# Kernel optimization log

Measured on AMD Instinct MI355X. Metric: run time of the kernel, lower is better.

## Reference

```python
import jax, jax.numpy as jnp
import numpy as np

N_HEAD = 16
N_EMBED = 1024

def setup_inputs() -> dict:
    key = jax.random.key(0)
    ks = jax.random.split(key, 5)
    C = N_EMBED
    x = jax.random.normal(ks[0], (2, 2048, C), dtype=jnp.float32)
    # c_attn: Linear(C, 3C); c_proj: Linear(C, C). PyTorch Linear: y = x @ W.T + b
    w_attn = jax.random.normal(ks[1], (3 * C, C), dtype=jnp.float32) * (1.0 / np.sqrt(C))
    b_attn = jnp.zeros((3 * C,), dtype=jnp.float32)
    w_proj = jax.random.normal(ks[2], (C, C), dtype=jnp.float32) * (1.0 / np.sqrt(C))
    b_proj = jnp.zeros((C,), dtype=jnp.float32)
    return {"x": x, "w_attn": w_attn, "b_attn": b_attn, "w_proj": w_proj, "b_proj": b_proj}

def reference(x, w_attn, b_attn, w_proj, b_proj):
    B, T, C = x.shape
    H = N_HEAD
    D = C // H
    qkv = jnp.einsum('btc,fc->btf', x, w_attn) + b_attn  # [B,T,3C]
    q, k, v = jnp.split(qkv, 3, axis=-1)
    # [B,H,T,D]
    q = q.reshape(B, T, H, D).transpose(0, 2, 1, 3)
    k = k.reshape(B, T, H, D).transpose(0, 2, 1, 3)
    v = v.reshape(B, T, H, D).transpose(0, 2, 1, 3)
    att = jnp.einsum('bhqd,bhkd->bhqk', q, k) * (1.0 / np.sqrt(D))  # [B,H,T,T]
    causal = jnp.tril(jnp.ones((T, T), dtype=bool))
    att = jnp.where(causal[None, None], att, jnp.finfo(att.dtype).min)
    att = jax.nn.softmax(att, axis=-1)
    y = jnp.einsum('bhqk,bhkd->bhqd', att, v)  # [B,H,T,D]
    y = y.transpose(0, 2, 1, 3).reshape(B, T, C)
    return jnp.einsum('btc,fc->btf', y, w_proj) + b_proj
```

## Files before the change

### kernel.cpp

```cpp
#include <hip/hip_runtime.h>
#include <hip/hip_bf16.h>

typedef unsigned short u16;
typedef __attribute__((ext_vector_type(8))) short v8s;
typedef __attribute__((ext_vector_type(4))) short v4s;
typedef __attribute__((ext_vector_type(4))) float v4f;

__device__ __forceinline__ u16 f2bu(float f) {
  union { float f; unsigned u; } v; v.f = f;
  unsigned r = (v.u + 0x7fffu + ((v.u >> 16) & 1u)) >> 16;
  return (u16)r;
}
__device__ __forceinline__ v4s pack4(const v4f& a) {
  union { v4s s; __hip_bfloat162 h[2]; } u;
  u.h[0] = __float22bfloat162_rn(make_float2(a[0], a[1]));
  u.h[1] = __float22bfloat162_rn(make_float2(a[2], a[3]));
  return u.s;
}
__device__ __forceinline__ v8s pack8(const v4f& a, const v4f& b) {
  union { v8s s; __hip_bfloat162 h[4]; } u;
  u.h[0] = __float22bfloat162_rn(make_float2(a[0], a[1]));
  u.h[1] = __float22bfloat162_rn(make_float2(a[2], a[3]));
  u.h[2] = __float22bfloat162_rn(make_float2(b[0], b[1]));
  u.h[3] = __float22bfloat162_rn(make_float2(b[2], b[3]));
  return u.s;
}

__device__ __forceinline__ void g2l16(const u16* g, u16* l) {
  __builtin_amdgcn_global_load_lds((const __attribute__((address_space(1))) void*)g,
                                   (__attribute__((address_space(3))) void*)l,
                                   16, 0, 0);
}

__global__ __launch_bounds__(256) void cvt_bf16(const float* __restrict__ s0, u16* __restrict__ d0, int n0,
                                                const float* __restrict__ s1, u16* __restrict__ d1, int n1,
                                                const float* __restrict__ s2, u16* __restrict__ d2, int n2) {
  int total8 = (n0 + n1 + n2) >> 3;
  for (int i = blockIdx.x * blockDim.x + threadIdx.x; i < total8; i += gridDim.x * blockDim.x) {
    int e = i << 3;
    const float* s; u16* d;
    if (e < n0)            { s = s0 + e;            d = d0 + e; }
    else if (e < n0 + n1)  { s = s1 + (e - n0);     d = d1 + (e - n0); }
    else                   { s = s2 + (e - n0 - n1); d = d2 + (e - n0 - n1); }
    v4f a = *(const v4f*)s, b = *(const v4f*)(s + 4);
    *(v8s*)d = pack8(a, b);
  }
}

template <int MODE>
__global__ __launch_bounds__(256) void gemm_bt(const u16* __restrict__ A,
                                               const u16* __restrict__ W,
                                               const float* __restrict__ bias,
                                               u16* __restrict__ o0,
                                               u16* __restrict__ o1,
                                               u16* __restrict__ o2,
                                               float* __restrict__ of) {
  constexpr int K = 1024;
  __shared__ __align__(16) u16 As[128 * 64];
  __shared__ __align__(16) u16 Bs[128 * 64];
  const int tid = threadIdx.x;
  const int w = tid >> 6, lane = tid & 63, l15 = lane & 15, quad = lane >> 4;
  const int wm = w & 1, wn = w >> 1;
  const int R0 = blockIdx.x * 128, C0 = blockIdx.y * 128;

  v4f acc[4][4] = {};
  const u16* Ag = A + (size_t)R0 * K;
  const u16* Wg = W + (size_t)C0 * K;

  int srow[4], scol[4], sdst[4];
#pragma unroll
  for (int i = 0; i < 4; ++i) {
    int p = (w * 4 + i) * 64 + lane;
    srow[i] = p >> 3;
    scol[i] = (p & 7) * 8;
    sdst[i] = (w * 4 + i) * 512;
  }

  for (int k0 = 0; k0 < K; k0 += 64) {
    if (k0) __syncthreads();
#pragma unroll
    for (int i = 0; i < 4; ++i) g2l16(Ag + srow[i] * K + k0 + scol[i], &As[sdst[i]]);
#pragma unroll
    for (int i = 0; i < 4; ++i) g2l16(Wg + srow[i] * K + k0 + scol[i], &Bs[sdst[i]]);
    __syncthreads();
#pragma unroll
    for (int kk = 0; kk < 2; ++kk) {
      v8s a[4], b[4];
#pragma unroll
      for (int m = 0; m < 4; ++m)
        a[m] = *(const v8s*)&As[(wm * 64 + m * 16 + l15) * 64 + (kk * 4 + quad) * 8];
#pragma unroll
      for (int n = 0; n < 4; ++n)
        b[n] = *(const v8s*)&Bs[(wn * 64 + n * 16 + l15) * 64 + (kk * 4 + quad) * 8];
#pragma unroll
      for (int m = 0; m < 4; ++m)
#pragma unroll
        for (int n = 0; n < 4; ++n)
          acc[m][n] = __builtin_amdgcn_mfma_f32_16x16x32_bf16(a[m], b[n], acc[m][n], 0, 0, 0);
    }
  }

#pragma unroll
  for (int n = 0; n < 4; ++n) {
    int f = C0 + wn * 64 + n * 16 + l15;
    float bv = bias[f];
#pragma unroll
    for (int m = 0; m < 4; ++m) {
      int r0 = R0 + wm * 64 + m * 16 + quad * 4;
      if (MODE == 1) {
#pragma unroll
        for (int reg = 0; reg < 4; ++reg)
          of[(size_t)(r0 + reg) * 1024 + f] = acc[m][n][reg] + bv;
      } else {
        int which = f >> 10, c = f & 1023;
        int h = c >> 6, d = c & 63;
        int b = r0 >> 11, t = r0 & 2047;
        if (which == 2) {
          v4s pk;
#pragma unroll
          for (int reg = 0; reg < 4; ++reg) pk[reg] = (short)f2bu(acc[m][n][reg] + bv);
          *(v4s*)&o2[(((b << 4) + h) * 64 + d) * 2048 + t] = pk;
        } else {
          u16* dst = (which == 0) ? o0 : o1;
#pragma unroll
          for (int reg = 0; reg < 4; ++reg)
            dst[(((b << 4) + h) * 2048 + (t + reg)) * 64 + d] = f2bu(acc[m][n][reg] + bv);
        }
      }
    }
  }
}

#define SCL2 0.180336879f
__global__ __launch_bounds__(256, 2) void attn_kernel(const u16* __restrict__ Q,
                                                      const u16* __restrict__ Kt,
                                                      const u16* __restrict__ Vt,
                                                      u16* __restrict__ Y) {
  __shared__ __align__(16) u16 Ksh[64 * 64], Vsh[64 * 64];
  __shared__ __align__(16) u16 Psh[8 * 16 * 72];
  const int tid = threadIdx.x;
  const int w = tid >> 6, lane = tid & 63, l15 = lane & 15, quad = lane >> 4;
  const int pi = blockIdx.x, h = blockIdx.y, b = blockIdx.z;
  const int qtA = pi, qtB = 31 - pi;
  const int qA0 = qtA * 64, qB0 = qtB * 64;
  const int bh = b * 16 + h;
  const u16* qg = Q + bh * 131072;
  const u16* kg = Kt + bh * 131072;
  const u16* vg = Vt + bh * 131072;

  v8s aqA[2], aqB[2];
  {
    const u16* qrA = qg + (qA0 + w * 16 + l15) * 64;
    const u16* qrB = qg + (qB0 + w * 16 + l15) * 64;
#pragma unroll
    for (int kk = 0; kk < 2; ++kk) {
      aqA[kk] = *(const v8s*)(qrA + kk * 32 + quad * 8);
      aqB[kk] = *(const v8s*)(qrB + kk * 32 + quad * 8);
    }
  }

  v4f OA[4] = {}, OB[4] = {};
  float llA = 0.f, llB = 0.f;
  const int rowlim = w * 16 + l15;

  int srow[2], sgc[2], ssc[2];
  v8s tk[2], tv[2];
#pragma unroll
  for (int i = 0; i < 2; ++i) {
    int cc = (w * 2 + i) * 64 + lane;
    srow[i] = cc >> 3; int c = cc & 7;
    sgc[i] = c * 8; ssc[i] = ((c ^ (srow[i] & 7)) * 8);
    tk[i] = *(const v8s*)(kg + srow[i] * 64 + sgc[i]);
    tv[i] = *(const v8s*)(vg + srow[i] * 2048 + sgc[i]);
  }

  u16* PA = &Psh[(w * 2) * 16 * 72];
  u16* PB = &Psh[(w * 2 + 1) * 16 * 72];

  for (int kt = 0; kt <= qtB; ++kt) {
    const int k0 = kt * 64;
    if (kt) __syncthreads();
#pragma unroll
    for (int i = 0; i < 2; ++i) {
      *(v8s*)&Ksh[srow[i] * 64 + ssc[i]] = tk[i];
      *(v8s*)&Vsh[srow[i] * 64 + ssc[i]] = tv[i];
    }
    __syncthreads();
    if (kt < qtB) {
      int kn = k0 + 64;
#pragma unroll
      for (int i = 0; i < 2; ++i) {
        tk[i] = *(const v8s*)(kg + (kn + srow[i]) * 64 + sgc[i]);
        tv[i] = *(const v8s*)(vg + srow[i] * 2048 + kn + sgc[i]);
      }
    }
    const bool doA = (kt <= qtA);

    v4f sA[4], sB[4];
#pragma unroll
    for (int nt = 0; nt < 4; ++nt) {
      v4f zb = {0.f, 0.f, 0.f, 0.f}, za = {0.f, 0.f, 0.f, 0.f};
#pragma unroll
      for (int kk = 0; kk < 2; ++kk) {
        v8s kf = *(const v8s*)&Ksh[(nt * 16 + l15) * 64 + (((kk * 4 + quad) ^ (l15 & 7)) * 8)];
        zb = __builtin_amdgcn_mfma_f32_16x16x32_bf16(kf, aqB[kk], zb, 0, 0, 0);
        if (doA) za = __builtin_amdgcn_mfma_f32_16x16x32_bf16(kf, aqA[kk], za, 0, 0, 0);
      }
      sB[nt] = zb; sA[nt] = za;
    }

    {
      float rs = 0.f;
      if (kt == qtB) {
#pragma unroll
        for (int nt = 0; nt < 4; ++nt)
#pragma unroll
          for (int reg = 0; reg < 4; ++reg) {
            int kl = nt * 16 + quad * 4 + reg;
            float p = (kl <= rowlim) ? exp2f(sB[nt][reg] * SCL2) : 0.f;
            sB[nt][reg] = p; rs += p;
          }
      } else {
#pragma unroll
        for (int nt = 0; nt < 4; ++nt)
#pragma unroll
          for (int reg = 0; reg < 4; ++reg) {
            float p = exp2f(sB[nt][reg] * SCL2);
            sB[nt][reg] = p; rs += p;
          }
      }
      llB += rs;
#pragma unroll
      for (int nt = 0; nt < 4; ++nt)
        *(v4s*)&PB[l15 * 72 + nt * 16 + quad * 4] = pack4(sB[nt]);
    }
    if (doA) {
      float rs = 0.f;
      if (kt == qtA) {
#pragma unroll
        for (int nt = 0; nt < 4; ++nt)
#pragma unroll
          for (int reg = 0; reg < 4; ++reg) {
            int kl = nt * 16 + quad * 4 + reg;
            float p = (kl <= rowlim) ? exp2f(sA[nt][reg] * SCL2) : 0.f;
            sA[nt][reg] = p; rs += p;
          }
      } else {
#pragma unroll
        for (int nt = 0; nt < 4; ++nt)
#pragma unroll
          for (int reg = 0; reg < 4; ++reg) {
            float p = exp2f(sA[nt][reg] * SCL2);
            sA[nt][reg] = p; rs += p;
          }
      }
      llA += rs;
#pragma unroll
      for (int nt = 0; nt < 4; ++nt)
        *(v4s*)&PA[l15 * 72 + nt * 16 + quad * 4] = pack4(sA[nt]);
    }

    asm volatile("" ::: "memory");
    v8s apB[2], apA[2];
#pragma unroll
    for (int kk = 0; kk < 2; ++kk) {
      apB[kk] = *(const v8s*)&PB[l15 * 72 + kk * 32 + quad * 8];
      if (doA) apA[kk] = *(const v8s*)&PA[l15 * 72 + kk * 32 + quad * 8];
    }
#pragma unroll
    for (int nt = 0; nt < 4; ++nt)
#pragma unroll
      for (int kk = 0; kk < 2; ++kk) {
        v8s vf = *(const v8s*)&Vsh[(nt * 16 + l15) * 64 + (((kk * 4 + quad) ^ (l15 & 7)) * 8)];
        OB[nt] = __builtin_amdgcn_mfma_f32_16x16x32_bf16(apB[kk], vf, OB[nt], 0, 0, 0);
        if (doA) OA[nt] = __builtin_amdgcn_mfma_f32_16x16x32_bf16(apA[kk], vf, OA[nt], 0, 0, 0);
      }
  }

  llB += __shfl_xor(llB, 16, 64); llB += __shfl_xor(llB, 32, 64);
  llA += __shfl_xor(llA, 16, 64); llA += __shfl_xor(llA, 32, 64);
  {
    float li = 1.f / llB, lO[4];
#pragma unroll
    for (int reg = 0; reg < 4; ++reg) lO[reg] = __shfl(li, quad * 4 + reg, 64);
    int tb2 = qB0 + w * 16 + quad * 4;
#pragma unroll
    for (int nt = 0; nt < 4; ++nt)
#pragma unroll
      for (int reg = 0; reg < 4; ++reg)
        Y[(b * 2048 + tb2 + reg) * 1024 + h * 64 + nt * 16 + l15] = f2bu(OB[nt][reg] * lO[reg]);
  }
  {
    float li = 1.f / llA, lO[4];
#pragma unroll
    for (int reg = 0; reg < 4; ++reg) lO[reg] = __shfl(li, quad * 4 + reg, 64);
    int tb2 = qA0 + w * 16 + quad * 4;
#pragma unroll
    for (int nt = 0; nt < 4; ++nt)
#pragma unroll
      for (int reg = 0; reg < 4; ++reg)
        Y[(b * 2048 + tb2 + reg) * 1024 + h * 64 + nt * 16 + l15] = f2bu(OA[nt][reg] * lO[reg]);
  }
}

extern "C" void kernel_launch(void* const* d_in, const int* in_sizes, int n_in,
                              void* d_out, int out_size, void* d_ws, size_t ws_size,
                              hipStream_t stream) {
  const float* x      = (const float*)d_in[0];
  const float* w_attn = (const float*)d_in[1];
  const float* b_attn = (const float*)d_in[2];
  const float* w_proj = (const float*)d_in[3];
  const float* b_proj = (const float*)d_in[4];
  float* out = (float*)d_out;
  char* ws = (char*)d_ws;
  u16* xb  = (u16*)(ws);
  u16* wab = (u16*)(ws + (size_t)( 8u << 20));
  u16* wpb = (u16*)(ws + (size_t)(14u << 20));
  u16* q   = (u16*)(ws + (size_t)(16u << 20));
  u16* k   = (u16*)(ws + (size_t)(24u << 20));
  u16* vt  = (u16*)(ws + (size_t)(32u << 20));
  u16* y   = (u16*)(ws + (size_t)(40u << 20));

  cvt_bf16<<<2048, 256, 0, stream>>>(x, xb, 4194304, w_attn, wab, 3145728, w_proj, wpb, 1048576);
  gemm_bt<0><<<dim3(32, 24), 256, 0, stream>>>(xb, wab, b_attn, q, k, vt, nullptr);
  attn_kernel<<<dim3(16, 16, 2), 256, 0, stream>>>(q, k, vt, y);
  gemm_bt<1><<<dim3(32, 8), 256, 0, stream>>>(y, wpb, b_proj, nullptr, nullptr, nullptr, out);
}
```

Baseline: 189.9 us.

## Double-buffer K/V tiles in attention and narrow proj GEMM tiles

The attention kernel now alternates between two K/V shared-memory buffers, which removes the leading barrier of each key-tile iteration. The output projection becomes its own kernel with 128x64 tiles, doubling its grid from 256 to 512 blocks so more CUs are filled. The cost is more LDS in attention, which may reduce occupancy, and more redundant A-tile loads in the projection.

```diff
diff --git a/kernel.cpp b/kernel.cpp
--- a/kernel.cpp
+++ b/kernel.cpp
@@ -47,14 +47,12 @@
   }
 }
 
-template <int MODE>
-__global__ __launch_bounds__(256) void gemm_bt(const u16* __restrict__ A,
-                                               const u16* __restrict__ W,
-                                               const float* __restrict__ bias,
-                                               u16* __restrict__ o0,
-                                               u16* __restrict__ o1,
-                                               u16* __restrict__ o2,
-                                               float* __restrict__ of) {
+__global__ __launch_bounds__(256) void gemm_qkv(const u16* __restrict__ A,
+                                                const u16* __restrict__ W,
+                                                const float* __restrict__ bias,
+                                                u16* __restrict__ o0,
+                                                u16* __restrict__ o1,
+                                                u16* __restrict__ o2) {
   constexpr int K = 1024;
   __shared__ __align__(16) u16 As[128 * 64];
   __shared__ __align__(16) u16 Bs[128 * 64];
@@ -107,26 +105,87 @@
 #pragma unroll
     for (int m = 0; m < 4; ++m) {
       int r0 = R0 + wm * 64 + m * 16 + quad * 4;
-      if (MODE == 1) {
+      int which = f >> 10, c = f & 1023;
+      int h = c >> 6, d = c & 63;
+      int b = r0 >> 11, t = r0 & 2047;
+      if (which == 2) {
+        v4s pk;
+#pragma unroll
+        for (int reg = 0; reg < 4; ++reg) pk[reg] = (short)f2bu(acc[m][n][reg] + bv);
+        *(v4s*)&o2[(((b << 4) + h) * 64 + d) * 2048 + t] = pk;
+      } else {
+        u16* dst = (which == 0) ? o0 : o1;
 #pragma unroll
         for (int reg = 0; reg < 4; ++reg)
-          of[(size_t)(r0 + reg) * 1024 + f] = acc[m][n][reg] + bv;
-      } else {
-        int which = f >> 10, c = f & 1023;
-        int h = c >> 6, d = c & 63;
-        int b = r0 >> 11, t = r0 & 2047;
-        if (which == 2) {
-          v4s pk;
-#pragma unroll
-          for (int reg = 0; reg < 4; ++reg) pk[reg] = (short)f2bu(acc[m][n][reg] + bv);
-          *(v4s*)&o2[(((b << 4) + h) * 64 + d) * 2048 + t] = pk;
-        } else {
-          u16* dst = (which == 0) ? o0 : o1;
-#pragma unroll
-          for (int reg = 0; reg < 4; ++reg)
-            dst[(((b << 4) + h) * 2048 + (t + reg)) * 64 + d] = f2bu(acc[m][n][reg] + bv);
-        }
-      }
+          dst[(((b << 4) + h) * 2048 + (t + reg)) * 64 + d] = f2bu(acc[m][n][reg] + bv);
+      }
+    }
+  }
+}
+
+__global__ __launch_bounds__(256) void gemm_proj(const u16* __restrict__ A,
+                                                 const u16* __restrict__ W,
+                                                 const float* __restrict__ bias,
+                                                 float* __restrict__ out) {
+  constexpr int K = 1024;
+  __shared__ __align__(16) u16 As[128 * 64];
+  __shared__ __align__(16) u16 Bs[64 * 64];
+  const int tid = threadIdx.x;
+  const int w = tid >> 6, lane = tid & 63, l15 = lane & 15, quad = lane >> 4;
+  const int wm = w & 1, wn = w >> 1;
+  const int R0 = blockIdx.x * 128, C0 = blockIdx.y * 64;
+
+  v4f acc[4][2] = {};
+  const u16* Ag = A + (size_t)R0 * K;
+  const u16* Wg = W + (size_t)C0 * K;
+
+  int arow[4], acol[4], adst[4];
+#pragma unroll
+  for (int i = 0; i < 4; ++i) {
+    int p = (w * 4 + i) * 64 + lane;
+    arow[i] = p >> 3; acol[i] = (p & 7) * 8; adst[i] = (w * 4 + i) * 512;
+  }
+  int brow[2], bcol[2], bdst[2];
+#pragma unroll
+  for (int i = 0; i < 2; ++i) {
+    int p = (w * 2 + i) * 64 + lane;
+    brow[i] = p >> 3; bcol[i] = (p & 7) * 8; bdst[i] = (w * 2 + i) * 512;
+  }
+
+  for (int k0 = 0; k0 < K; k0 += 64) {
+    if (k0) __syncthreads();
+#pragma unroll
+    for (int i = 0; i < 4; ++i) g2l16(Ag + arow[i] * K + k0 + acol[i], &As[adst[i]]);
+#pragma unroll
+    for (int i = 0; i < 2; ++i) g2l16(Wg + brow[i] * K + k0 + bcol[i], &Bs[bdst[i]]);
+    __syncthreads();
+#pragma unroll
+    for (int kk = 0; kk < 2; ++kk) {
+      v8s a[4], b[2];
+#pragma unroll
+      for (int m = 0; m < 4; ++m)
+        a[m] = *(const v8s*)&As[(wm * 64 + m * 16 + l15) * 64 + (kk * 4 + quad) * 8];
+#pragma unroll
+      for (int n = 0; n < 2; ++n)
+        b[n] = *(const v8s*)&Bs[(wn * 32 + n * 16 + l15) * 64 + (kk * 4 + quad) * 8];
+#pragma unroll
+      for (int m = 0; m < 4; ++m)
+#pragma unroll
+        for (int n = 0; n < 2; ++n)
+          acc[m][n] = __builtin_amdgcn_mfma_f32_16x16x32_bf16(a[m], b[n], acc[m][n], 0, 0, 0);
+    }
+  }
+
+#pragma unroll
+  for (int n = 0; n < 2; ++n) {
+    int f = C0 + wn * 32 + n * 16 + l15;
+    float bv = bias[f];
+#pragma unroll
+    for (int m = 0; m < 4; ++m) {
+      int r0 = R0 + wm * 64 + m * 16 + quad * 4;
+#pragma unroll
+      for (int reg = 0; reg < 4; ++reg)
+        out[(size_t)(r0 + reg) * 1024 + f] = acc[m][n][reg] + bv;
     }
   }
 }
@@ -136,7 +195,7 @@
                                                       const u16* __restrict__ Kt,
                                                       const u16* __restrict__ Vt,
                                                       u16* __restrict__ Y) {
-  __shared__ __align__(16) u16 Ksh[64 * 64], Vsh[64 * 64];
+  __shared__ __align__(16) u16 Ksh[2][64 * 64], Vsh[2][64 * 64];
   __shared__ __align__(16) u16 Psh[8 * 16 * 72];
   const int tid = threadIdx.x;
   const int w = tid >> 6, lane = tid & 63, l15 = lane & 15, quad = lane >> 4;
@@ -179,11 +238,11 @@
 
   for (int kt = 0; kt <= qtB; ++kt) {
     const int k0 = kt * 64;
-    if (kt) __syncthreads();
+    const int buf = kt & 1;
 #pragma unroll
     for (int i = 0; i < 2; ++i) {
-      *(v8s*)&Ksh[srow[i] * 64 + ssc[i]] = tk[i];
-      *(v8s*)&Vsh[srow[i] * 64 + ssc[i]] = tv[i];
+      *(v8s*)&Ksh[buf][srow[i] * 64 + ssc[i]] = tk[i];
+      *(v8s*)&Vsh[buf][srow[i] * 64 + ssc[i]] = tv[i];
     }
     __syncthreads();
     if (kt < qtB) {
@@ -195,6 +254,8 @@
       }
     }
     const bool doA = (kt <= qtA);
+    const u16* Kb = Ksh[buf];
+    const u16* Vb = Vsh[buf];
 
     v4f sA[4], sB[4];
 #pragma unroll
@@ -202,7 +263,7 @@
       v4f zb = {0.f, 0.f, 0.f, 0.f}, za = {0.f, 0.f, 0.f, 0.f};
 #pragma unroll
       for (int kk = 0; kk < 2; ++kk) {
-        v8s kf = *(const v8s*)&Ksh[(nt * 16 + l15) * 64 + (((kk * 4 + quad) ^ (l15 & 7)) * 8)];
+        v8s kf = *(const v8s*)&Kb[(nt * 16 + l15) * 64 + (((kk * 4 + quad) ^ (l15 & 7)) * 8)];
         zb = __builtin_amdgcn_mfma_f32_16x16x32_bf16(kf, aqB[kk], zb, 0, 0, 0);
         if (doA) za = __builtin_amdgcn_mfma_f32_16x16x32_bf16(kf, aqA[kk], za, 0, 0, 0);
       }
@@ -271,7 +332,7 @@
     for (int nt = 0; nt < 4; ++nt)
 #pragma unroll
       for (int kk = 0; kk < 2; ++kk) {
-        v8s vf = *(const v8s*)&Vsh[(nt * 16 + l15) * 64 + (((kk * 4 + quad) ^ (l15 & 7)) * 8)];
+        v8s vf = *(const v8s*)&Vb[(nt * 16 + l15) * 64 + (((kk * 4 + quad) ^ (l15 & 7)) * 8)];
         OB[nt] = __builtin_amdgcn_mfma_f32_16x16x32_bf16(apB[kk], vf, OB[nt], 0, 0, 0);
         if (doA) OA[nt] = __builtin_amdgcn_mfma_f32_16x16x32_bf16(apA[kk], vf, OA[nt], 0, 0, 0);
       }
@@ -322,7 +383,7 @@
   u16* y   = (u16*)(ws + (size_t)(40u << 20));
 
   cvt_bf16<<<2048, 256, 0, stream>>>(x, xb, 4194304, w_attn, wab, 3145728, w_proj, wpb, 1048576);
-  gemm_bt<0><<<dim3(32, 24), 256, 0, stream>>>(xb, wab, b_attn, q, k, vt, nullptr);
+  gemm_qkv<<<dim3(32, 24), 256, 0, stream>>>(xb, wab, b_attn, q, k, vt);
   attn_kernel<<<dim3(16, 16, 2), 256, 0, stream>>>(q, k, vt, y);
-  gemm_bt<1><<<dim3(32, 8), 256, 0, stream>>>(y, wpb, b_proj, nullptr, nullptr, nullptr, out);
-}
+  gemm_proj<<<dim3(32, 16), 256, 0, stream>>>(y, wpb, b_proj, out);
+}
```

New measurement: 186.5 us. No clear change (-1.8%).
